# Optimization experiments

Measured on AMD Instinct MI355X. Metric: run time of the kernel, lower is better.

Reference implementation:

```python
import jax, jax.numpy as jnp
import numpy as np

N, CIN, COUT, K, S, H, W = 16, 512, 512, 3, 512, 64, 64
EPS = 1e-8


def setup_inputs() -> dict:
    key = jax.random.key(0)
    k1, k2, k3, k4 = jax.random.split(key, 4)
    return {
        "x": jax.random.normal(k1, (N, CIN, H, W), jnp.float32),
        "style": jax.random.normal(k2, (N, S), jnp.float32),
        # conv weight ~ N(0,1) as in the torch module (lr_mul=1)
        "weight": jax.random.normal(k3, (COUT, CIN, K, K), jnp.float32),
        # style modulation linear: weight ~ N(0,1), bias init 1.0
        "style_w": jax.random.normal(k4, (CIN, S), jnp.float32),
        "style_b": jnp.ones((CIN,), jnp.float32),
    }


def reference(x, style, weight, style_w, style_b):
    # equalized-lr scales (gain=1.0, lr_mul=1.0, mode=fan_in)
    lin_scale = 1.0 / jnp.sqrt(jnp.float32(S))          # fan_in of linear = style_channels
    w_scale = 1.0 / jnp.sqrt(jnp.float32(CIN * K * K))  # fan_in of weight[0] = Cin*k*k

    # style modulation: s[n, cin] (style_bias = 0.0)
    s = style @ (style_w.T * lin_scale) + style_b        # [N, Cin]

    w = weight * w_scale                                  # [Cout, Cin, K, K]

    # demodulation: rsqrt(sum_{i,kh,kw} (w[o,i]*s[n,i])^2 + eps) per (n, o)
    demod = jax.lax.rsqrt(jnp.einsum('oikl,ni->no', w * w, s * s) + EPS)  # [N, Cout]

    # fused form: conv(x * s, W) * demod  ==  grouped conv with per-sample modulated weights
    xs = x * s[:, :, None, None]
    out = jax.lax.conv_general_dilated(
        xs, w, window_strides=(1, 1), padding='SAME',
        dimension_numbers=('NCHW', 'OIHW', 'NCHW'))
    return out * demod[:, :, None, None]
```

## Files before the change

kernel.cpp:

```cpp
#include <hip/hip_runtime.h>
#include <hip/hip_bf16.h>

#define CIN   512
#define COUT  512
#define HW    4096
#define PADW  66
#define NB    16
#define KTOT  4608
#define BUFSZ 65536
#define BOFF  32768

static constexpr float LIN_SCALE = 0.044194173824159216f;
static constexpr float W_SCALE   = 0.014731391274719738f;

typedef __attribute__((ext_vector_type(8))) short bf16x8;
typedef __attribute__((ext_vector_type(4))) float f32x4;

__device__ __forceinline__ unsigned short f2us(float f) {
    __hip_bfloat16 h = __float2bfloat16(f); unsigned short u; __builtin_memcpy(&u, &h, 2); return u;
}

typedef const __attribute__((address_space(1))) unsigned int guint;
typedef __attribute__((address_space(3))) unsigned int luint;
__device__ __forceinline__ void gload_lds16(const void* g, void* l) {
    __builtin_amdgcn_global_load_lds((guint*)g, (luint*)l, 16, 0, 0);
}

__global__ void k_style(const float* __restrict__ style,
                        const float* __restrict__ style_w,
                        const float* __restrict__ style_b,
                        float* __restrict__ s) {
    int wid  = (blockIdx.x * blockDim.x + threadIdx.x) >> 6;
    int lane = threadIdx.x & 63;
    int n = wid >> 9, i = wid & 511;
    float sum = 0.f;
    for (int j = lane; j < 512; j += 64)
        sum += style[n * 512 + j] * style_w[i * 512 + j];
    for (int m = 32; m; m >>= 1) sum += __shfl_xor(sum, m, 64);
    if (lane == 0) s[n * 512 + i] = sum * LIN_SCALE + style_b[i];
}

__global__ void k_wprep(const float* __restrict__ weight,
                        float* __restrict__ wsq,
                        __hip_bfloat16* __restrict__ wt) {
    int oi = blockIdx.x * 256 + threadIdx.x;
    int o = oi >> 9, i = oi & 511;
    float sq = 0.f;
#pragma unroll
    for (int tp = 0; tp < 9; ++tp) {
        float v = weight[(size_t)oi * 9 + tp] * W_SCALE;
        sq += v * v;
        wt[(size_t)o * KTOT + tp * 512 + i] = __float2bfloat16(v);
    }
    wsq[oi] = sq;
}

__global__ void k_demod(const float* __restrict__ wsq, const float* __restrict__ s,
                        float* __restrict__ demod) {
    int wid  = (blockIdx.x * blockDim.x + threadIdx.x) >> 6;
    int lane = threadIdx.x & 63;
    int n = wid >> 9, o = wid & 511;
    float sum = 0.f;
    for (int i = lane; i < 512; i += 64) {
        float sv = s[n * 512 + i];
        sum += wsq[o * 512 + i] * sv * sv;
    }
    for (int m = 32; m; m >>= 1) sum += __shfl_xor(sum, m, 64);
    if (lane == 0) demod[n * 512 + o] = rsqrtf(sum + 1e-8f);
}

__global__ void k_border(__hip_bfloat16* __restrict__ xs) {
    int bp = blockIdx.x, n = blockIdx.y, t = threadIdx.x;
    int hp, wp;
    if (bp < 66)       { hp = 0;  wp = bp; }
    else if (bp < 132) { hp = 65; wp = bp - 66; }
    else { int k2 = bp - 132; hp = 1 + (k2 >> 1); wp = (k2 & 1) ? 65 : 0; }
    uint4 z = make_uint4(0u, 0u, 0u, 0u);
    *(uint4*)(xs + (((size_t)n * PADW * PADW) + hp * PADW + wp) * 512 + t * 8) = z;
}

__global__ void k_xs(const float* __restrict__ x, const float* __restrict__ s,
                     __hip_bfloat16* __restrict__ xs) {
    const int h = blockIdx.x;
    const int n = blockIdx.y;
    const int t = threadIdx.x;
    const int PITCH = 66;
    __shared__ float lds[64 * 66];
    for (int ic = 0; ic < 8; ++ic) {
        const int i0 = ic * 64;
        __syncthreads();
#pragma unroll
        for (int j = 0; j < 4; ++j) {
            int idx = j * 256 + t;
            int il = idx >> 4;
            int wq = (idx & 15) * 4;
            float4 v = *(const float4*)(x + (((size_t)n * 512 + i0 + il) * HW) + h * 64 + wq);
            float* dst = &lds[il * PITCH + wq];
            dst[0] = v.x; dst[1] = v.y; dst[2] = v.z; dst[3] = v.w;
        }
        __syncthreads();
#pragma unroll
        for (int j = 0; j < 2; ++j) {
            int idx = j * 256 + t;
            int wp = idx >> 3;
            int ib = (idx & 7) * 8;
            unsigned short tmp[8];
#pragma unroll
            for (int r = 0; r < 8; ++r) {
                float xv = lds[(ib + r) * PITCH + wp];
                float sv = s[n * 512 + i0 + ib + r];
                tmp[r] = f2us(xv * sv);
            }
            uint4 o;
            o.x = (unsigned)tmp[0] | ((unsigned)tmp[1] << 16);
            o.y = (unsigned)tmp[2] | ((unsigned)tmp[3] << 16);
            o.z = (unsigned)tmp[4] | ((unsigned)tmp[5] << 16);
            o.w = (unsigned)tmp[6] | ((unsigned)tmp[7] << 16);
            *(uint4*)(xs + ((size_t)((n * PADW + h + 1) * PADW + (wp + 1))) * 512 + i0 + ib) = o;
        }
    }
}

#define BAR      __builtin_amdgcn_s_barrier()
#define WAITLGKM asm volatile("s_waitcnt lgkmcnt(0)" ::: "memory")
#define LOAD_B(CH) { _Pragma("unroll") for (int t_ = 0; t_ < 4; ++t_) \
    bfr[t_] = *(const bf16x8*)(cb + BOFF + bRow + t_ * 2048 + (CH)); }
#define LOAD_A(MG, CH) { _Pragma("unroll") for (int t_ = 0; t_ < 4; ++t_) \
    af[t_] = *(const bf16x8*)(cb + aRow + ((MG) * 4 + t_) * 2048 + (CH)); }
#define DO_MFMA(MG) { __builtin_amdgcn_s_setprio(1); \
    _Pragma("unroll") for (int m_ = 0; m_ < 4; ++m_) \
    _Pragma("unroll") for (int n_ = 0; n_ < 4; ++n_) \
        acc[(MG) * 4 + m_][n_] = __builtin_amdgcn_mfma_f32_16x16x32_bf16( \
            af[m_], bfr[n_], acc[(MG) * 4 + m_][n_], 0, 0, 0); \
    __builtin_amdgcn_s_setprio(0); }

__global__ __launch_bounds__(512, 2) void k_conv(
        const __hip_bfloat16* __restrict__ wt,
        const __hip_bfloat16* __restrict__ xs,
        const float* __restrict__ demod,
        float* __restrict__ out) {
    __shared__ __attribute__((aligned(16))) char smem[2 * BUFSZ];
    const int tid  = threadIdx.x;
    const int wv   = tid >> 6, lane = tid & 63;
    const int wm   = wv >> 2,  wn   = wv & 3;

    const int bid = blockIdx.x;
    const int xcd = bid & 7, idx = bid >> 3;
    const int pT  = idx & 15;
    const int o0  = ((idx >> 4) & 1) * 256;
    const int smp = xcd * 2 + (idx >> 5);

    const __hip_bfloat16* xsn = xs + (size_t)smp * (PADW * PADW * 512);

    const int rw = lane >> 3, cl = lane & 7;
    const int lc = cl ^ rw;
    const size_t aOff = (size_t)(wv * 8 + rw) * KTOT + lc * 8;
    const size_t bOff = (size_t)(wv * 8 + rw) * 512  + lc * 8;
    const __hip_bfloat16* aStage = wt  + (size_t)o0 * KTOT + aOff;
    const __hip_bfloat16* bStage = xsn + bOff;

    const int col = lane & 15, qd = lane >> 4;
    const int ch0 = ((qd)     ^ (col & 7)) << 4;
    const int ch1 = ((qd + 4) ^ (col & 7)) << 4;
    const int aRow = (wm * 128 + col) * 128;
    const int bRow = (wn * 64  + col) * 128;

    f32x4 acc[8][4] = {};

    {
        char* nbB = smem + BOFF + wv * 1024;
        char* nbA = smem + wv * 1024;
        const __hip_bfloat16* bS = bStage + (size_t)(pT * 4) * 33792;
        gload_lds16(bS,              nbB);
        gload_lds16(bS + 33792,      nbB + 8192);
        gload_lds16(bS + 2 * 33792,  nbB + 2 * 8192);
        gload_lds16(bS + 3 * 33792,  nbB + 3 * 8192);
        gload_lds16(aStage,              nbA);
        gload_lds16(aStage + 2 * 294912, nbA + 2 * 8192);
        gload_lds16(aStage + 294912,     nbA + 8192);
        gload_lds16(aStage + 3 * 294912, nbA + 3 * 8192);
        asm volatile("s_waitcnt vmcnt(2)" ::: "memory");
        BAR;
    }

    for (int kt = 0; kt < 71; ++kt) {
        char* cb = smem + (kt & 1) * BUFSZ;
        char* nb = smem + ((kt + 1) & 1) * BUFSZ;
        const int kt1  = kt + 1;
        const int tap1 = kt1 >> 3, c1 = kt1 & 7;
        const int kh1  = tap1 / 3, kw1 = tap1 - kh1 * 3;
        const __hip_bfloat16* aS = aStage + (size_t)kt1 * 64;
        const __hip_bfloat16* bS = bStage +
            (size_t)((pT * 4 + kh1) * PADW + kw1) * 512 + c1 * 64;
        char* nbB = nb + BOFF + wv * 1024;
        char* nbA = nb + wv * 1024;

        bf16x8 af[4], bfr[4];

        LOAD_B(ch0); LOAD_A(0, ch0);
        gload_lds16(bS,             nbB);
        gload_lds16(bS + 33792,     nbB + 8192);
        gload_lds16(bS + 2 * 33792, nbB + 2 * 8192);
        BAR; WAITLGKM;
        DO_MFMA(0);
        asm volatile("s_waitcnt vmcnt(3)" ::: "memory");
        BAR;

        LOAD_A(1, ch0);
        gload_lds16(bS + 3 * 33792, nbB + 3 * 8192);
        gload_lds16(aS,             nbA);
        gload_lds16(aS + 2 * 294912, nbA + 2 * 8192);
        BAR; WAITLGKM;
        DO_MFMA(1);
        BAR;

        LOAD_B(ch1); LOAD_A(0, ch1);
        gload_lds16(aS + 294912,     nbA + 8192);
        gload_lds16(aS + 3 * 294912, nbA + 3 * 8192);
        BAR; WAITLGKM;
        DO_MFMA(0);
        BAR;

        LOAD_A(1, ch1);
        BAR; WAITLGKM;
        DO_MFMA(1);
        asm volatile("s_waitcnt vmcnt(2)" ::: "memory");
        BAR;
    }

    {
        char* cb = smem + BUFSZ;
        asm volatile("s_waitcnt vmcnt(0)" ::: "memory");
        BAR;
        bf16x8 af[4], bfr[4];
        LOAD_B(ch0); LOAD_A(0, ch0); DO_MFMA(0);
        LOAD_A(1, ch0);              DO_MFMA(1);
        LOAD_B(ch1); LOAD_A(0, ch1); DO_MFMA(0);
        LOAD_A(1, ch1);              DO_MFMA(1);
    }

    const int hwBase = pT * 256 + wn * 64 + col;
#pragma unroll
    for (int m = 0; m < 8; ++m) {
#pragma unroll
        for (int rg = 0; rg < 4; ++rg) {
            const int o = o0 + wm * 128 + m * 16 + qd * 4 + rg;
            const float dm = demod[smp * 512 + o];
            float* orow = out + ((size_t)(smp * COUT + o)) * HW + hwBase;
#pragma unroll
            for (int nn = 0; nn < 4; ++nn)
                orow[nn * 16] = acc[m][nn][rg] * dm;
        }
    }
}

extern "C" void kernel_launch(void* const* d_in, const int* in_sizes, int n_in,
                              void* d_out, int out_size, void* d_ws, size_t ws_size,
                              hipStream_t stream) {
    const float* x       = (const float*)d_in[0];
    const float* style   = (const float*)d_in[1];
    const float* weight  = (const float*)d_in[2];
    const float* style_w = (const float*)d_in[3];
    const float* style_b = (const float*)d_in[4];
    float* out = (float*)d_out;

    char* ws = (char*)d_ws;
    float*          s_buf  = (float*)(ws + 0);
    float*          wsq    = (float*)(ws + 32768);
    float*          demod  = (float*)(ws + 1081344);
    __hip_bfloat16* wt     = (__hip_bfloat16*)(ws + 1114112);
    __hip_bfloat16* xs     = (__hip_bfloat16*)(ws + 5832704);

    k_style <<<dim3(2048),     dim3(256), 0, stream>>>(style, style_w, style_b, s_buf);
    k_wprep <<<dim3(1024),     dim3(256), 0, stream>>>(weight, wsq, wt);
    k_demod <<<dim3(2048),     dim3(256), 0, stream>>>(wsq, s_buf, demod);
    k_border<<<dim3(260, 16),  dim3(64),  0, stream>>>(xs);
    k_xs    <<<dim3(64, 16),   dim3(256), 0, stream>>>(x, s_buf, xs);
    k_conv  <<<dim3(512),      dim3(512), 0, stream>>>(wt, xs, demod, out);
}
```

Baseline: 503.3 us.

## Restructure conv LDS/MFMA pipeline, fuse border zeroing into xs prep

Reworks the conv main loop to preload more fragments into separate registers (A groups and both B channels) and uses partial lgkmcnt waits with sched barriers so MFMA groups can start while later LDS reads are still in flight. Global-to-LDS prefetches are regrouped and a full vmcnt(0) wait is now done at iteration end. Also folds the border-zeroing kernel into k_xs as an extra block column, caches s in LDS, and changes the LDS pitch to 65 to reduce bank conflicts. These trade higher register pressure and a stricter vmcnt wait for fewer launches and better LDS/MFMA overlap.

```diff
diff --git a/kernel.cpp b/kernel.cpp
--- a/kernel.cpp
+++ b/kernel.cpp
@@ -69,23 +69,28 @@
     if (lane == 0) demod[n * 512 + o] = rsqrtf(sum + 1e-8f);
 }
 
-__global__ void k_border(__hip_bfloat16* __restrict__ xs) {
-    int bp = blockIdx.x, n = blockIdx.y, t = threadIdx.x;
-    int hp, wp;
-    if (bp < 66)       { hp = 0;  wp = bp; }
-    else if (bp < 132) { hp = 65; wp = bp - 66; }
-    else { int k2 = bp - 132; hp = 1 + (k2 >> 1); wp = (k2 & 1) ? 65 : 0; }
-    uint4 z = make_uint4(0u, 0u, 0u, 0u);
-    *(uint4*)(xs + (((size_t)n * PADW * PADW) + hp * PADW + wp) * 512 + t * 8) = z;
-}
-
 __global__ void k_xs(const float* __restrict__ x, const float* __restrict__ s,
                      __hip_bfloat16* __restrict__ xs) {
-    const int h = blockIdx.x;
     const int n = blockIdx.y;
     const int t = threadIdx.x;
-    const int PITCH = 66;
-    __shared__ float lds[64 * 66];
+    if (blockIdx.x == 64) {
+        uint4 z = make_uint4(0u, 0u, 0u, 0u);
+        for (int idx = t; idx < 16640; idx += 256) {
+            int bp = idx >> 6, sl = idx & 63;
+            int hp, wp;
+            if (bp < 66)       { hp = 0;  wp = bp; }
+            else if (bp < 132) { hp = 65; wp = bp - 66; }
+            else { int k2 = bp - 132; hp = 1 + (k2 >> 1); wp = (k2 & 1) ? 65 : 0; }
+            *(uint4*)(xs + (((size_t)n * PADW * PADW) + hp * PADW + wp) * 512 + sl * 8) = z;
+        }
+        return;
+    }
+    const int h = blockIdx.x;
+    const int PITCH = 65;
+    __shared__ float lds[64 * 65];
+    __shared__ float sv[512];
+    sv[t] = s[n * 512 + t];
+    sv[t + 256] = s[n * 512 + 256 + t];
     for (int ic = 0; ic < 8; ++ic) {
         const int i0 = ic * 64;
         __syncthreads();
@@ -108,8 +113,7 @@
 #pragma unroll
             for (int r = 0; r < 8; ++r) {
                 float xv = lds[(ib + r) * PITCH + wp];
-                float sv = s[n * 512 + i0 + ib + r];
-                tmp[r] = f2us(xv * sv);
+                tmp[r] = f2us(xv * sv[i0 + ib + r]);
             }
             uint4 o;
             o.x = (unsigned)tmp[0] | ((unsigned)tmp[1] << 16);
@@ -121,17 +125,17 @@
     }
 }
 
-#define BAR      __builtin_amdgcn_s_barrier()
-#define WAITLGKM asm volatile("s_waitcnt lgkmcnt(0)" ::: "memory")
-#define LOAD_B(CH) { _Pragma("unroll") for (int t_ = 0; t_ < 4; ++t_) \
-    bfr[t_] = *(const bf16x8*)(cb + BOFF + bRow + t_ * 2048 + (CH)); }
-#define LOAD_A(MG, CH) { _Pragma("unroll") for (int t_ = 0; t_ < 4; ++t_) \
-    af[t_] = *(const bf16x8*)(cb + aRow + ((MG) * 4 + t_) * 2048 + (CH)); }
-#define DO_MFMA(MG) { __builtin_amdgcn_s_setprio(1); \
+#define BAR __builtin_amdgcn_s_barrier()
+#define SB0 __builtin_amdgcn_sched_barrier(0)
+#define LD_B(dst, CH) { _Pragma("unroll") for (int t_ = 0; t_ < 4; ++t_) \
+    dst[t_] = *(const bf16x8*)(cb + BOFF + bRow + t_ * 2048 + (CH)); }
+#define LD_A(dst, MG, CH) { _Pragma("unroll") for (int t_ = 0; t_ < 4; ++t_) \
+    dst[t_] = *(const bf16x8*)(cb + aRow + ((MG) * 4 + t_) * 2048 + (CH)); }
+#define MFMA_G(MG, AF, BF) { __builtin_amdgcn_s_setprio(1); \
     _Pragma("unroll") for (int m_ = 0; m_ < 4; ++m_) \
     _Pragma("unroll") for (int n_ = 0; n_ < 4; ++n_) \
         acc[(MG) * 4 + m_][n_] = __builtin_amdgcn_mfma_f32_16x16x32_bf16( \
-            af[m_], bfr[n_], acc[(MG) * 4 + m_][n_], 0, 0, 0); \
+            AF[m_], BF[n_], acc[(MG) * 4 + m_][n_], 0, 0, 0); \
     __builtin_amdgcn_s_setprio(0); }
 
 __global__ __launch_bounds__(512, 2) void k_conv(
@@ -176,15 +180,15 @@
         gload_lds16(bS + 2 * 33792,  nbB + 2 * 8192);
         gload_lds16(bS + 3 * 33792,  nbB + 3 * 8192);
         gload_lds16(aStage,              nbA);
+        gload_lds16(aStage + 294912,     nbA + 8192);
         gload_lds16(aStage + 2 * 294912, nbA + 2 * 8192);
-        gload_lds16(aStage + 294912,     nbA + 8192);
         gload_lds16(aStage + 3 * 294912, nbA + 3 * 8192);
-        asm volatile("s_waitcnt vmcnt(2)" ::: "memory");
+        asm volatile("s_waitcnt vmcnt(0)" ::: "memory");
         BAR;
     }
 
     for (int kt = 0; kt < 71; ++kt) {
-        char* cb = smem + (kt & 1) * BUFSZ;
+        const char* cb = smem + (kt & 1) * BUFSZ;
         char* nb = smem + ((kt + 1) & 1) * BUFSZ;
         const int kt1  = kt + 1;
         const int tap1 = kt1 >> 3, c1 = kt1 & 7;
@@ -195,48 +199,47 @@
         char* nbB = nb + BOFF + wv * 1024;
         char* nbA = nb + wv * 1024;
 
-        bf16x8 af[4], bfr[4];
-
-        LOAD_B(ch0); LOAD_A(0, ch0);
+        bf16x8 bf0[4], bf1[4], afA[4], afB[4];
+
+        LD_B(bf0, ch0); LD_A(afA, 0, ch0); LD_A(afB, 1, ch0);
         gload_lds16(bS,             nbB);
         gload_lds16(bS + 33792,     nbB + 8192);
         gload_lds16(bS + 2 * 33792, nbB + 2 * 8192);
-        BAR; WAITLGKM;
-        DO_MFMA(0);
-        asm volatile("s_waitcnt vmcnt(3)" ::: "memory");
-        BAR;
-
-        LOAD_A(1, ch0);
         gload_lds16(bS + 3 * 33792, nbB + 3 * 8192);
-        gload_lds16(aS,             nbA);
+        BAR;
+        asm volatile("s_waitcnt lgkmcnt(4)" ::: "memory"); SB0;
+        MFMA_G(0, afA, bf0);
+        BAR;
+
+        LD_B(bf1, ch1); LD_A(afA, 0, ch1);
+        gload_lds16(aS,              nbA);
+        gload_lds16(aS + 294912,     nbA + 8192);
         gload_lds16(aS + 2 * 294912, nbA + 2 * 8192);
-        BAR; WAITLGKM;
-        DO_MFMA(1);
-        BAR;
-
-        LOAD_B(ch1); LOAD_A(0, ch1);
-        gload_lds16(aS + 294912,     nbA + 8192);
         gload_lds16(aS + 3 * 294912, nbA + 3 * 8192);
-        BAR; WAITLGKM;
-        DO_MFMA(0);
-        BAR;
-
-        LOAD_A(1, ch1);
-        BAR; WAITLGKM;
-        DO_MFMA(1);
-        asm volatile("s_waitcnt vmcnt(2)" ::: "memory");
+        BAR;
+        asm volatile("s_waitcnt lgkmcnt(8)" ::: "memory"); SB0;
+        MFMA_G(1, afB, bf0);
+        BAR;
+
+        LD_A(afB, 1, ch1);
+        BAR;
+        asm volatile("s_waitcnt lgkmcnt(4)" ::: "memory"); SB0;
+        MFMA_G(0, afA, bf1);
+        BAR;
+
+        asm volatile("s_waitcnt lgkmcnt(0)" ::: "memory"); SB0;
+        MFMA_G(1, afB, bf1);
+        asm volatile("s_waitcnt vmcnt(0)" ::: "memory");
         BAR;
     }
 
     {
-        char* cb = smem + BUFSZ;
-        asm volatile("s_waitcnt vmcnt(0)" ::: "memory");
-        BAR;
-        bf16x8 af[4], bfr[4];
-        LOAD_B(ch0); LOAD_A(0, ch0); DO_MFMA(0);
-        LOAD_A(1, ch0);              DO_MFMA(1);
-        LOAD_B(ch1); LOAD_A(0, ch1); DO_MFMA(0);
-        LOAD_A(1, ch1);              DO_MFMA(1);
+        const char* cb = smem + BUFSZ;
+        bf16x8 bf0[4], bf1[4], afA[4], afB[4];
+        LD_B(bf0, ch0); LD_A(afA, 0, ch0); MFMA_G(0, afA, bf0);
+        LD_A(afB, 1, ch0);                 MFMA_G(1, afB, bf0);
+        LD_B(bf1, ch1); LD_A(afA, 0, ch1); MFMA_G(0, afA, bf1);
+        LD_A(afB, 1, ch1);                 MFMA_G(1, afB, bf1);
     }
 
     const int hwBase = pT * 256 + wn * 64 + col;
@@ -274,7 +277,6 @@
     k_style <<<dim3(2048),     dim3(256), 0, stream>>>(style, style_w, style_b, s_buf);
     k_wprep <<<dim3(1024),     dim3(256), 0, stream>>>(weight, wsq, wt);
     k_demod <<<dim3(2048),     dim3(256), 0, stream>>>(wsq, s_buf, demod);
-    k_border<<<dim3(260, 16),  dim3(64),  0, stream>>>(xs);
-    k_xs    <<<dim3(64, 16),   dim3(256), 0, stream>>>(x, s_buf, xs);
+    k_xs    <<<dim3(65, 16),   dim3(256), 0, stream>>>(x, s_buf, xs);
     k_conv  <<<dim3(512),      dim3(512), 0, stream>>>(wt, xs, demod, out);
 }
```

New measurement: 512.3 us. Within noise of the previous version (+1.8%).
